# Kernel optimization log

Hardware: AMD Instinct MI355X
Metric: run time of the kernel (lower is better)

The kernel has to match this reference:

```python
import jax, jax.numpy as jnp
import numpy as np

NU, NI, NA, D = 100000, 100000, 10000, 64
N0 = NU + NI        # user+item graph nodes
N1 = NU + NA        # user+author graph nodes
E0, E1, E3, E4, E5 = 6_400_000, 3_520_000, 1_000_000, 1_000_000, 2_000_000
N_LAYERS = 3
EPS = 1e-12


def setup_inputs() -> dict:
    key = jax.random.key(0)
    ks = jax.random.split(key, 18)
    inp = {
        'emb_user': 0.1 * jax.random.normal(ks[0], (NU, D), jnp.float32),
        'emb_item': 0.1 * jax.random.normal(ks[1], (NI, D), jnp.float32),
        'emb_author': 0.1 * jax.random.normal(ks[2], (NA, D), jnp.float32),
        'g0_row': jax.random.randint(ks[3], (E0,), 0, N0, jnp.int32),
        'g0_col': jax.random.randint(ks[4], (E0,), 0, N0, jnp.int32),
        'g0_val': jax.random.uniform(ks[5], (E0,), jnp.float32) / 32.0,
        'g1_row': jax.random.randint(ks[6], (E1,), 0, N1, jnp.int32),
        'g1_col': jax.random.randint(ks[7], (E1,), 0, N1, jnp.int32),
        'g1_val': jax.random.uniform(ks[8], (E1,), jnp.float32) / 32.0,
        'g3_row': jax.random.randint(ks[9], (E3,), 0, NA, jnp.int32),
        'g3_col': jax.random.randint(ks[10], (E3,), 0, NI, jnp.int32),
        'g3_val': jax.random.uniform(ks[11], (E3,), jnp.float32),
        'g4_row': jax.random.randint(ks[12], (E4,), 0, NI, jnp.int32),
        'g4_col': jax.random.randint(ks[13], (E4,), 0, NA, jnp.int32),
        'g4_val': jax.random.uniform(ks[14], (E4,), jnp.float32),
        'g5_row': jax.random.randint(ks[15], (E5,), 0, NI, jnp.int32),
        'g5_col': jax.random.randint(ks[16], (E5,), 0, NI, jnp.int32),
        'g5_val': jax.random.uniform(ks[17], (E5,), jnp.float32),
    }
    return inp


def _spmm(row, col, val, x, n):
    # sparse [n, m] @ dense [m, d] via gather + segment_sum
    return jax.ops.segment_sum(val[:, None] * x[col], row, num_segments=n)


def _normalize(x):
    # F.normalize(x, p=2, dim=1)
    return x / jnp.maximum(jnp.linalg.norm(x, axis=1, keepdims=True), EPS)


def _one_propagate(row, col, val, a, b, n):
    # LightGCN propagation: stack per-layer features, mean across layers
    feats = jnp.concatenate([a, b], axis=0)  # [n, D]
    acc = feats
    cur = feats
    for _ in range(N_LAYERS):
        cur = _spmm(row, col, val, cur, n)
        acc = acc + cur
    out = acc / (N_LAYERS + 1)
    return out[: a.shape[0]], out[a.shape[0]:]


def reference(emb_user, emb_item, emb_author,
              g0_row, g0_col, g0_val,
              g1_row, g1_col, g1_val,
              g3_row, g3_col, g3_val,
              g4_row, g4_col, g4_val,
              g5_row, g5_col, g5_val):
    # atom branch: user-item graph
    atom_users, atom_items0 = _one_propagate(g0_row, g0_col, g0_val, emb_user, emb_item, N0)
    atom_authors = _normalize(_spmm(g3_row, g3_col, g3_val, atom_items0, NA))
    atom_items = 0.5 * _normalize(_spmm(g5_row, g5_col, g5_val, atom_items0, NI)) + 0.5 * atom_items0
    # non-atom branch: user-author graph
    non_atom_users, non_atom_authors = _one_propagate(g1_row, g1_col, g1_val, emb_user, emb_author, N1)
    non_atom_items = _normalize(_spmm(g4_row, g4_col, g4_val, non_atom_authors, NI))
    # computer() returns ([u0,u1],[i0,i1],[a0,a1]); concat to one array for a single baseline output
    return jnp.concatenate([atom_users, non_atom_users,
                            atom_items, non_atom_items,
                            atom_authors, non_atom_authors], axis=0)
```

## Files before the change

### kernel.cpp

```cpp
#include <hip/hip_runtime.h>

#define NUu 100000
#define NIi 100000
#define NAa 10000
#define DD  64
#define NN0 (NUu + NIi)
#define NN1 (NUu + NAa)

typedef unsigned int uint;
typedef unsigned short ushort;


__device__ __forceinline__ uint pack_bf2(float x, float y) {
    uint a = __float_as_uint(x);
    uint b = __float_as_uint(y);
    a = (a + 0x7fffu + ((a >> 16) & 1u)) >> 16;
    b = (b + 0x7fffu + ((b >> 16) & 1u)) & 0xffff0000u;
    return (a & 0xffffu) | b;
}
__device__ __forceinline__ float bflo(uint w) { return __uint_as_float(w << 16); }
__device__ __forceinline__ float bfhi(uint w) { return __uint_as_float(w & 0xffff0000u); }

__device__ __forceinline__ uint enc14(float v) {
    uint u = __float_as_uint(v);
    uint bf = (u + 0x7fffu + ((u >> 16) & 1u)) >> 16;
    return ((bf + 1u) >> 1) & 0x3FFFu;
}
__device__ __forceinline__ float dec14(uint e) { return __uint_as_float(e << 17); }

__global__ void k_f2bf3(const float4* __restrict__ su, const float4* __restrict__ si,
                        const float4* __restrict__ sa,
                        uint2* __restrict__ du, uint2* __restrict__ di,
                        uint2* __restrict__ da) {
    int i = blockIdx.x * blockDim.x + threadIdx.x;
    const int nu = NUu * 16, ni = NIi * 16, na = NAa * 16;
    const float4* s;
    uint2* d;
    int j;
    if (i < nu) { s = su; d = du; j = i; }
    else if (i < nu + ni) { s = si; d = di; j = i - nu; }
    else if (i < nu + ni + na) { s = sa; d = da; j = i - nu - ni; }
    else return;
    float4 v = s[j];
    uint2 o;
    o.x = pack_bf2(v.x, v.y);
    o.y = pack_bf2(v.z, v.w);
    d[j] = o;
}


#define P1_ITER 8
#define SEG_CAP 9472

__global__ void k_arenainit(int* __restrict__ bc,
                            int nb0, int nb1, int nb2, int nb3, int nb4,
                            int c0, int c1, int c2, int c3, int c4) {
    int t = threadIdx.x;
    if (t < nb0) bc[t] = t * c0;
    if (t < nb1) bc[1024 + t] = t * c1;
    if (t < nb2) bc[2048 + t] = t * c2;
    if (t < nb3) bc[3072 + t] = t * c3;
    if (t < nb4) bc[4096 + t] = t * c4;
}

__global__ void __launch_bounds__(1024)
k_part1(const int* __restrict__ row, const int* __restrict__ col,
        const float* __restrict__ val, int* __restrict__ binCur,
        int2* __restrict__ stage, int E, int shift, int nbins, int cap) {
    __shared__ int h[1024];
    for (int t = threadIdx.x; t < nbins; t += blockDim.x) h[t] = 0;
    __syncthreads();
    int e0 = blockIdx.x * (blockDim.x * P1_ITER) + threadIdx.x;
    int r[P1_ITER];
#pragma unroll
    for (int i = 0; i < P1_ITER; ++i) {
        int e = e0 + i * blockDim.x;
        r[i] = (e < E) ? row[e] : -1;
        if (r[i] >= 0) atomicAdd(&h[r[i] >> shift], 1);
    }
    __syncthreads();
    for (int t = threadIdx.x; t < nbins; t += blockDim.x) {
        int c = h[t];
        h[t] = c ? atomicAdd(binCur + t, c) : 0;
    }
    __syncthreads();
#pragma unroll
    for (int i = 0; i < P1_ITER; ++i) {
        int e = e0 + i * blockDim.x;
        if (e < E) {
            int rr = r[i];
            int b = rr >> shift;
            int pos = atomicAdd(&h[b], 1);
            if (pos < (b + 1) * cap) {
                int2 p;
                p.x = ((rr & ((1 << shift) - 1)) << 18) | col[e];
                p.y = __float_as_int(val[e]);
                stage[pos] = p;
            }
        }
    }
}

__global__ void __launch_bounds__(1024)
k_part2(const int* __restrict__ binCur, const int2* __restrict__ stage,
        uint* __restrict__ csr, int2* __restrict__ rp2, int N, int shift, int cap) {
    __shared__ int2 seg[SEG_CAP];
    __shared__ int h[512];
    __shared__ int s[512];
    int tid = threadIdx.x;
    int rbase = blockIdx.x << shift;
    int nr = min(1 << shift, N - rbase);
    int es = blockIdx.x * cap;
    int ee = min(binCur[blockIdx.x], es + cap);
    int n = ee - es;
    if (tid < 512) h[tid] = 0;
    for (int i = tid; i < n; i += blockDim.x) seg[i] = stage[es + i];
    __syncthreads();
    for (int i = tid; i < n; i += blockDim.x)
        atomicAdd(&h[seg[i].x >> 18], 1);
    __syncthreads();
    int v = (tid < 512) ? h[tid] : 0;
    if (tid < 512) s[tid] = v;
    __syncthreads();
    for (int off = 1; off < 512; off <<= 1) {
        int t = (tid < 512 && tid >= off) ? s[tid - off] : 0;
        __syncthreads();
        if (tid < 512) s[tid] += t;
        __syncthreads();
    }
    if (tid < 512) h[tid] = es + s[tid] - v;
    if (tid < nr) {
        int st = es + s[tid] - v;
        rp2[rbase + tid] = make_int2(st, st + v);
    }
    __syncthreads();
    for (int i = tid; i < n; i += blockDim.x) {
        int2 p = seg[i];
        int pos = atomicAdd(&h[p.x >> 18], 1);
        csr[pos] = (((uint)(p.x & 0x3ffff)) << 14) | enc14(__int_as_float(p.y));
    }
}


template <bool SS>
__device__ __forceinline__ const uint* gb(uint pe, const uint* xbA, const uint* xbB,
                                          int split) {
    int c = (int)(pe >> 14);
    if (SS) return (c < split) ? xbA + (((long long)c) << 5)
                               : xbB + (((long long)(c - split)) << 5);
    return xbA + (((long long)c) << 5);
}

template <int MODE, bool SS>
__global__ void k_spmm(const int2* __restrict__ rp2, const uint* __restrict__ csr,
                       const uint* __restrict__ xbA, const uint* __restrict__ xbB, int split,
                       const float* __restrict__ embA, const float* __restrict__ embB,
                       const uint* __restrict__ y1b, const uint* __restrict__ y2b,
                       float* __restrict__ outU, float* __restrict__ outI,
                       uint* __restrict__ outIb,
                       uint* __restrict__ ob, float* __restrict__ yf,
                       const float* __restrict__ base, int nrows) {
    int r = blockIdx.x * (blockDim.x >> 6) + (threadIdx.x >> 6);
    if (r >= nrows) return;
    int lane = threadIdx.x & 63;
    int q = lane >> 4;
    int d8 = lane & 15;

    int2 se = rp2[r];
    int s0 = se.x, e0 = se.y;
    float a0 = 0.f, a1 = 0.f, a2 = 0.f, a3 = 0.f;
    int i = s0;
    for (; i + 32 <= e0; i += 32) {
        uint pe[8];
#pragma unroll
        for (int s = 0; s < 8; ++s)
            pe[s] = csr[i + 4 * s + q];
        uint2 wv[8];
#pragma unroll
        for (int s = 0; s < 8; ++s)
            wv[s] = *(const uint2*)(gb<SS>(pe[s], xbA, xbB, split) + 2 * d8);
#pragma unroll
        for (int s = 0; s < 8; ++s) {
            float v = dec14(pe[s] & 0x3FFFu);
            a0 += v * bflo(wv[s].x); a1 += v * bfhi(wv[s].x);
            a2 += v * bflo(wv[s].y); a3 += v * bfhi(wv[s].y);
        }
    }
    for (; i + 8 <= e0; i += 8) {
        uint p0 = csr[i + q];
        uint p1 = csr[i + 4 + q];
        uint2 w0 = *(const uint2*)(gb<SS>(p0, xbA, xbB, split) + 2 * d8);
        uint2 w1 = *(const uint2*)(gb<SS>(p1, xbA, xbB, split) + 2 * d8);
        float v0 = dec14(p0 & 0x3FFFu);
        float v1 = dec14(p1 & 0x3FFFu);
        a0 += v0 * bflo(w0.x); a1 += v0 * bfhi(w0.x);
        a2 += v0 * bflo(w0.y); a3 += v0 * bfhi(w0.y);
        a0 += v1 * bflo(w1.x); a1 += v1 * bfhi(w1.x);
        a2 += v1 * bflo(w1.y); a3 += v1 * bfhi(w1.y);
    }
    for (; i < e0; i += 4) {
        int idx = i + q;
        uint pe = (idx < e0) ? csr[idx] : 0u;
        uint2 wv = *(const uint2*)(gb<SS>(pe, xbA, xbB, split) + 2 * d8);
        float v = dec14(pe & 0x3FFFu);
        a0 += v * bflo(wv.x); a1 += v * bfhi(wv.x); a2 += v * bflo(wv.y); a3 += v * bfhi(wv.y);
    }
    a0 += __shfl_xor(a0, 16); a0 += __shfl_xor(a0, 32);
    a1 += __shfl_xor(a1, 16); a1 += __shfl_xor(a1, 32);
    a2 += __shfl_xor(a2, 16); a2 += __shfl_xor(a2, 32);
    a3 += __shfl_xor(a3, 16); a3 += __shfl_xor(a3, 32);

    long long off4 = (((long long)r) << 6) + 4 * d8;
    long long offw = (((long long)r) << 5) + 2 * d8;

    if (MODE == 0) {
        if (q == 0) {
            uint2 o;
            o.x = pack_bf2(a0, a1);
            o.y = pack_bf2(a2, a3);
            *(uint2*)(ob + offw) = o;
        }
    } else if (MODE == 1) {
        if (q == 0) {
            float4 e4;
            if (r < split) e4 = *(const float4*)(embA + off4);
            else           e4 = *(const float4*)(embB + (off4 - (((long long)split) << 6)));
            uint2 w1 = *(const uint2*)(y1b + offw);
            uint2 w2 = *(const uint2*)(y2b + offw);
            float s0f = 0.25f * (e4.x + bflo(w1.x) + bflo(w2.x) + a0);
            float s1f = 0.25f * (e4.y + bfhi(w1.x) + bfhi(w2.x) + a1);
            float s2f = 0.25f * (e4.z + bflo(w1.y) + bflo(w2.y) + a2);
            float s3f = 0.25f * (e4.w + bfhi(w1.y) + bfhi(w2.y) + a3);
            float4 o;
            o.x = s0f; o.y = s1f; o.z = s2f; o.w = s3f;
            if (r < split) {
                *(float4*)(outU + off4) = o;
            } else {
                *(float4*)(outI + (off4 - (((long long)split) << 6))) = o;
                if (outIb) {
                    uint2 ob2;
                    ob2.x = pack_bf2(s0f, s1f);
                    ob2.y = pack_bf2(s2f, s3f);
                    *(uint2*)(outIb + (((long long)(r - split)) << 5) + 2 * d8) = ob2;
                }
            }
        }
    } else {
        float sq = a0 * a0 + a1 * a1 + a2 * a2 + a3 * a3;
        sq += __shfl_xor(sq, 1); sq += __shfl_xor(sq, 2);
        sq += __shfl_xor(sq, 4); sq += __shfl_xor(sq, 8);
        float inv = 1.0f / fmaxf(sqrtf(sq), 1e-12f);
        if (q == 0) {
            float4 o;
            if (MODE == 2) {
                o.x = a0 * inv; o.y = a1 * inv; o.z = a2 * inv; o.w = a3 * inv;
            } else {
                float4 b4 = *(const float4*)(base + off4);
                o.x = 0.5f * a0 * inv + 0.5f * b4.x;
                o.y = 0.5f * a1 * inv + 0.5f * b4.y;
                o.z = 0.5f * a2 * inv + 0.5f * b4.z;
                o.w = 0.5f * a3 * inv + 0.5f * b4.w;
            }
            *(float4*)(yf + off4) = o;
        }
    }
}


static inline int nblk(long long n, int b) { return (int)((n + b - 1) / b); }
static inline size_t al256(size_t x) { return (x + 255) & ~(size_t)255; }
#define AMAX 7250000

extern "C" void kernel_launch(void* const* d_in, const int* in_sizes, int n_in,
                              void* d_out, int out_size, void* d_ws, size_t ws_size,
                              hipStream_t stream) {
    const float* emb_user   = (const float*)d_in[0];
    const float* emb_item   = (const float*)d_in[1];
    const float* emb_author = (const float*)d_in[2];
    const int*   g0r = (const int*)d_in[3];
    const int*   g0c = (const int*)d_in[4];
    const float* g0v = (const float*)d_in[5];
    const int*   g1r = (const int*)d_in[6];
    const int*   g1c = (const int*)d_in[7];
    const float* g1v = (const float*)d_in[8];
    const int*   g3r = (const int*)d_in[9];
    const int*   g3c = (const int*)d_in[10];
    const float* g3v = (const float*)d_in[11];
    const int*   g4r = (const int*)d_in[12];
    const int*   g4c = (const int*)d_in[13];
    const float* g4v = (const float*)d_in[14];
    const int*   g5r = (const int*)d_in[15];
    const int*   g5c = (const int*)d_in[16];
    const float* g5v = (const float*)d_in[17];

    const int E0 = in_sizes[3];
    const int E1 = in_sizes[6];
    const int E3 = in_sizes[9];
    const int E4 = in_sizes[12];
    const int E5 = in_sizes[15];

    float* out = (float*)d_out;

    char* w = (char*)d_ws;
    int2* rp2     = (int2*)w; w += al256((size_t)(NN0 + 1) * 8);
    int*  binCur5 = (int*)w;  w += al256((size_t)5 * 1024 * 4);
    uint* csr     = (uint*)w; w += al256((size_t)AMAX * 4);
    uint* embUb   = (uint*)w; w += al256((size_t)NUu * 32 * 4);
    uint* embIb   = (uint*)w; w += al256((size_t)NIi * 32 * 4);
    uint* embAb   = (uint*)w; w += al256((size_t)NAa * 32 * 4);
    uint* y1b     = (uint*)w; w += al256((size_t)NN0 * 32 * 4);
    uint* y2b     = (uint*)w; w += al256((size_t)NN0 * 32 * 4);
    uint* items0b = (uint*)w; w += al256((size_t)NIi * 32 * 4);
    float* items0 = (float*)w; w += al256((size_t)NIi * DD * 4);
    uint* oAuthNb = (uint*)w; w += al256((size_t)NAa * 32 * 4);
    int2* stage = (int2*)y1b;

    const int B = 256;

    struct G { int nbins, shift, cap; };
    auto geo = [](int E, int N, int shift) {
        G g;
        g.shift = shift;
        g.nbins = (N + (1 << shift) - 1) >> shift;
        int cap = E / g.nbins + E / (16 * g.nbins) + 512;
        g.cap = cap > SEG_CAP ? SEG_CAP : cap;
        return g;
    };
    G gg0 = geo(E0, NN0, 8), gg1 = geo(E1, NN1, 8), gg3 = geo(E3, NAa, 5),
      gg5 = geo(E5, NIi, 8), gg4 = geo(E4, NIi, 8);

    float* oUserA = out;
    float* oUserN = out + (long long)NUu * DD;
    float* oItemA = out + (long long)200000 * DD;
    float* oItemN = out + (long long)300000 * DD;
    float* oAuthA = out + (long long)400000 * DD;
    float* oAuthN = out + (long long)410000 * DD;

    k_f2bf3<<<nblk((long long)(NUu + NIi + NAa) * 16, B), B, 0, stream>>>(
        (const float4*)emb_user, (const float4*)emb_item, (const float4*)emb_author,
        (uint2*)embUb, (uint2*)embIb, (uint2*)embAb);
    k_arenainit<<<1, 1024, 0, stream>>>(binCur5,
        gg0.nbins, gg1.nbins, gg3.nbins, gg5.nbins, gg4.nbins,
        gg0.cap, gg1.cap, gg3.cap, gg5.cap, gg4.cap);

    auto build = [&](const int* row, const int* col, const float* val,
                     int E, int N, const G& g, int slot) {
        int* bc = binCur5 + slot * 1024;
        k_part1<<<nblk(E, 1024 * P1_ITER), 1024, 0, stream>>>(row, col, val, bc,
                                                              stage, E, g.shift,
                                                              g.nbins, g.cap);
        k_part2<<<g.nbins, 1024, 0, stream>>>(bc, stage, csr, rp2, N, g.shift, g.cap);
    };

    build(g0r, g0c, g0v, E0, NN0, gg0, 0);
    k_spmm<0, true><<<nblk(NN0, 4), B, 0, stream>>>(rp2, csr, embUb, embIb, NUu,
                                                    nullptr, nullptr, nullptr, nullptr,
                                                    nullptr, nullptr, nullptr,
                                                    y1b, nullptr, nullptr, NN0);
    k_spmm<0, false><<<nblk(NN0, 4), B, 0, stream>>>(rp2, csr, y1b, nullptr, 0,
                                                     nullptr, nullptr, nullptr, nullptr,
                                                     nullptr, nullptr, nullptr,
                                                     y2b, nullptr, nullptr, NN0);
    k_spmm<1, false><<<nblk(NN0, 4), B, 0, stream>>>(rp2, csr, y2b, nullptr, NUu,
                                                     emb_user, emb_item, y1b, y2b,
                                                     oUserA, items0, items0b,
                                                     nullptr, nullptr, nullptr, NN0);

    build(g1r, g1c, g1v, E1, NN1, gg1, 1);
    k_spmm<0, true><<<nblk(NN1, 4), B, 0, stream>>>(rp2, csr, embUb, embAb, NUu,
                                                    nullptr, nullptr, nullptr, nullptr,
                                                    nullptr, nullptr, nullptr,
                                                    y1b, nullptr, nullptr, NN1);
    k_spmm<0, false><<<nblk(NN1, 4), B, 0, stream>>>(rp2, csr, y1b, nullptr, 0,
                                                     nullptr, nullptr, nullptr, nullptr,
                                                     nullptr, nullptr, nullptr,
                                                     y2b, nullptr, nullptr, NN1);
    k_spmm<1, false><<<nblk(NN1, 4), B, 0, stream>>>(rp2, csr, y2b, nullptr, NUu,
                                                     emb_user, emb_author, y1b, y2b,
                                                     oUserN, oAuthN, oAuthNb,
                                                     nullptr, nullptr, nullptr, NN1);

    build(g3r, g3c, g3v, E3, NAa, gg3, 2);
    k_spmm<2, false><<<nblk(NAa, 4), B, 0, stream>>>(rp2, csr, items0b, nullptr, 0,
                                                     nullptr, nullptr, nullptr, nullptr,
                                                     nullptr, nullptr, nullptr,
                                                     nullptr, oAuthA, nullptr, NAa);

    build(g5r, g5c, g5v, E5, NIi, gg5, 3);
    k_spmm<3, false><<<nblk(NIi, 4), B, 0, stream>>>(rp2, csr, items0b, nullptr, 0,
                                                     nullptr, nullptr, nullptr, nullptr,
                                                     nullptr, nullptr, nullptr,
                                                     nullptr, oItemA, items0, NIi);

    build(g4r, g4c, g4v, E4, NIi, gg4, 4);
    k_spmm<2, false><<<nblk(NIi, 4), B, 0, stream>>>(rp2, csr, oAuthNb, nullptr, 0,
                                                     nullptr, nullptr, nullptr, nullptr,
                                                     nullptr, nullptr, nullptr,
                                                     nullptr, oItemN, nullptr, NIi);
}
```

Baseline: 1.076 ms.

## Split LightGCN propagation into two 32-column halves for cache-resident gathers

The bf16 embeddings and intermediate layer buffers are stored as two separate 32-column halves, and each 3-layer propagation runs twice, once per half, with a new half-width SpMM kernel. Halving the gathered row footprint is meant to let the randomly accessed source matrix fit better in L2/LLC and cut gather traffic. In exchange, the CSR index and value stream is read twice as often, kernel launches double, and each gather is now a 4-byte load per lane instead of 8.

```diff
diff --git a/kernel.cpp b/kernel.cpp
--- a/kernel.cpp
+++ b/kernel.cpp
@@ -28,24 +28,27 @@
 }
 __device__ __forceinline__ float dec14(uint e) { return __uint_as_float(e << 17); }
 
-__global__ void k_f2bf3(const float4* __restrict__ su, const float4* __restrict__ si,
-                        const float4* __restrict__ sa,
-                        uint2* __restrict__ du, uint2* __restrict__ di,
-                        uint2* __restrict__ da) {
+__global__ void k_f2bf3s(const float4* __restrict__ su, const float4* __restrict__ si,
+                         const float4* __restrict__ sa,
+                         uint2* __restrict__ ulo, uint2* __restrict__ uhi,
+                         uint2* __restrict__ ilo, uint2* __restrict__ ihi,
+                         uint2* __restrict__ alo, uint2* __restrict__ ahi) {
     int i = blockIdx.x * blockDim.x + threadIdx.x;
     const int nu = NUu * 16, ni = NIi * 16, na = NAa * 16;
     const float4* s;
-    uint2* d;
+    uint2 *dlo, *dhi;
     int j;
-    if (i < nu) { s = su; d = du; j = i; }
-    else if (i < nu + ni) { s = si; d = di; j = i - nu; }
-    else if (i < nu + ni + na) { s = sa; d = da; j = i - nu - ni; }
+    if (i < nu) { s = su; dlo = ulo; dhi = uhi; j = i; }
+    else if (i < nu + ni) { s = si; dlo = ilo; dhi = ihi; j = i - nu; }
+    else if (i < nu + ni + na) { s = sa; dlo = alo; dhi = ahi; j = i - nu - ni; }
     else return;
     float4 v = s[j];
     uint2 o;
     o.x = pack_bf2(v.x, v.y);
     o.y = pack_bf2(v.z, v.w);
-    d[j] = o;
+    int n = j >> 4, k = j & 15;
+    uint2* d = (k < 8) ? dlo : dhi;
+    d[n * 8 + (k & 7)] = o;
 }
 
 
@@ -141,25 +144,101 @@
     }
 }
 
-
-template <bool SS>
-__device__ __forceinline__ const uint* gb(uint pe, const uint* xbA, const uint* xbB,
-                                          int split) {
-    int c = (int)(pe >> 14);
-    if (SS) return (c < split) ? xbA + (((long long)c) << 5)
-                               : xbB + (((long long)(c - split)) << 5);
-    return xbA + (((long long)c) << 5);
-}
-
 template <int MODE, bool SS>
+__global__ void k_spmmh(const int2* __restrict__ rp2, const uint* __restrict__ csr,
+                        const uint* __restrict__ xbA, const uint* __restrict__ xbB,
+                        int split, int dOff,
+                        const float* __restrict__ embA, const float* __restrict__ embB,
+                        const uint* __restrict__ y1p, const uint* __restrict__ y2p,
+                        float* __restrict__ outU, float* __restrict__ outI,
+                        uint* __restrict__ outIb, uint* __restrict__ yp, int nrows) {
+    int r = blockIdx.x * (blockDim.x >> 6) + (threadIdx.x >> 6);
+    if (r >= nrows) return;
+    int lane = threadIdx.x & 63;
+    int q = lane >> 4;
+    int d8 = lane & 15;
+
+    int2 se = rp2[r];
+    int s0 = se.x, e0 = se.y;
+    float a0 = 0.f, a1 = 0.f;
+    int i = s0;
+    for (; i + 32 <= e0; i += 32) {
+        uint pe[8];
+#pragma unroll
+        for (int s = 0; s < 8; ++s)
+            pe[s] = csr[i + 4 * s + q];
+        uint wv[8];
+#pragma unroll
+        for (int s = 0; s < 8; ++s) {
+            int c = (int)(pe[s] >> 14);
+            const uint* b = SS ? ((c < split) ? xbA + (((long long)c) << 4)
+                                             : xbB + (((long long)(c - split)) << 4))
+                               : xbA + (((long long)c) << 4);
+            wv[s] = b[d8];
+        }
+#pragma unroll
+        for (int s = 0; s < 8; ++s) {
+            float v = dec14(pe[s] & 0x3FFFu);
+            a0 += v * bflo(wv[s]); a1 += v * bfhi(wv[s]);
+        }
+    }
+    for (; i + 8 <= e0; i += 8) {
+        uint p0 = csr[i + q];
+        uint p1 = csr[i + 4 + q];
+        int c0 = (int)(p0 >> 14), c1 = (int)(p1 >> 14);
+        const uint* b0 = SS ? ((c0 < split) ? xbA + (((long long)c0) << 4)
+                                            : xbB + (((long long)(c0 - split)) << 4))
+                            : xbA + (((long long)c0) << 4);
+        const uint* b1 = SS ? ((c1 < split) ? xbA + (((long long)c1) << 4)
+                                            : xbB + (((long long)(c1 - split)) << 4))
+                            : xbA + (((long long)c1) << 4);
+        uint w0 = b0[d8], w1 = b1[d8];
+        float v0 = dec14(p0 & 0x3FFFu);
+        float v1 = dec14(p1 & 0x3FFFu);
+        a0 += v0 * bflo(w0); a1 += v0 * bfhi(w0);
+        a0 += v1 * bflo(w1); a1 += v1 * bfhi(w1);
+    }
+    for (; i < e0; i += 4) {
+        int idx = i + q;
+        uint pe = (idx < e0) ? csr[idx] : 0u;
+        int c = (int)(pe >> 14);
+        const uint* b = SS ? ((c < split) ? xbA + (((long long)c) << 4)
+                                          : xbB + (((long long)(c - split)) << 4))
+                           : xbA + (((long long)c) << 4);
+        uint w = b[d8];
+        float v = dec14(pe & 0x3FFFu);
+        a0 += v * bflo(w); a1 += v * bfhi(w);
+    }
+    a0 += __shfl_xor(a0, 16); a0 += __shfl_xor(a0, 32);
+    a1 += __shfl_xor(a1, 16); a1 += __shfl_xor(a1, 32);
+
+    if (q != 0) return;
+    if (MODE == 0) {
+        yp[(((long long)r) << 4) + d8] = pack_bf2(a0, a1);
+    } else {
+        long long offf = (((long long)r) << 6) + dOff + 2 * d8;
+        float2 e2;
+        if (r < split) e2 = *(const float2*)(embA + offf);
+        else           e2 = *(const float2*)(embB + (offf - (((long long)split) << 6)));
+        uint w1 = y1p[(((long long)r) << 4) + d8];
+        uint w2 = y2p[(((long long)r) << 4) + d8];
+        float s0f = 0.25f * (e2.x + bflo(w1) + bflo(w2) + a0);
+        float s1f = 0.25f * (e2.y + bfhi(w1) + bfhi(w2) + a1);
+        float2 o; o.x = s0f; o.y = s1f;
+        if (r < split) {
+            *(float2*)(outU + offf) = o;
+        } else {
+            *(float2*)(outI + (offf - (((long long)split) << 6))) = o;
+            if (outIb)
+                outIb[(((long long)(r - split)) << 5) + (dOff >> 1) + d8] = pack_bf2(s0f, s1f);
+        }
+    }
+}
+
+template <int MODE>
 __global__ void k_spmm(const int2* __restrict__ rp2, const uint* __restrict__ csr,
-                       const uint* __restrict__ xbA, const uint* __restrict__ xbB, int split,
-                       const float* __restrict__ embA, const float* __restrict__ embB,
-                       const uint* __restrict__ y1b, const uint* __restrict__ y2b,
-                       float* __restrict__ outU, float* __restrict__ outI,
-                       uint* __restrict__ outIb,
-                       uint* __restrict__ ob, float* __restrict__ yf,
-                       const float* __restrict__ base, int nrows) {
+                       const uint* __restrict__ xb,
+                       float* __restrict__ yf, const float* __restrict__ base, int nrows) {
     int r = blockIdx.x * (blockDim.x >> 6) + (threadIdx.x >> 6);
     if (r >= nrows) return;
     int lane = threadIdx.x & 63;
@@ -178,7 +257,7 @@
         uint2 wv[8];
 #pragma unroll
         for (int s = 0; s < 8; ++s)
-            wv[s] = *(const uint2*)(gb<SS>(pe[s], xbA, xbB, split) + 2 * d8);
+            wv[s] = *(const uint2*)(xb + (((long long)(pe[s] >> 14)) << 5) + 2 * d8);
 #pragma unroll
         for (int s = 0; s < 8; ++s) {
             float v = dec14(pe[s] & 0x3FFFu);
@@ -186,22 +265,10 @@
             a2 += v * bflo(wv[s].y); a3 += v * bfhi(wv[s].y);
         }
     }
-    for (; i + 8 <= e0; i += 8) {
-        uint p0 = csr[i + q];
-        uint p1 = csr[i + 4 + q];
-        uint2 w0 = *(const uint2*)(gb<SS>(p0, xbA, xbB, split) + 2 * d8);
-        uint2 w1 = *(const uint2*)(gb<SS>(p1, xbA, xbB, split) + 2 * d8);
-        float v0 = dec14(p0 & 0x3FFFu);
-        float v1 = dec14(p1 & 0x3FFFu);
-        a0 += v0 * bflo(w0.x); a1 += v0 * bfhi(w0.x);
-        a2 += v0 * bflo(w0.y); a3 += v0 * bfhi(w0.y);
-        a0 += v1 * bflo(w1.x); a1 += v1 * bfhi(w1.x);
-        a2 += v1 * bflo(w1.y); a3 += v1 * bfhi(w1.y);
-    }
     for (; i < e0; i += 4) {
         int idx = i + q;
         uint pe = (idx < e0) ? csr[idx] : 0u;
-        uint2 wv = *(const uint2*)(gb<SS>(pe, xbA, xbB, split) + 2 * d8);
+        uint2 wv = *(const uint2*)(xb + (((long long)(pe >> 14)) << 5) + 2 * d8);
         float v = dec14(pe & 0x3FFFu);
         a0 += v * bflo(wv.x); a1 += v * bfhi(wv.x); a2 += v * bflo(wv.y); a3 += v * bfhi(wv.y);
     }
@@ -210,59 +277,23 @@
     a2 += __shfl_xor(a2, 16); a2 += __shfl_xor(a2, 32);
     a3 += __shfl_xor(a3, 16); a3 += __shfl_xor(a3, 32);
 
-    long long off4 = (((long long)r) << 6) + 4 * d8;
-    long long offw = (((long long)r) << 5) + 2 * d8;
-
-    if (MODE == 0) {
-        if (q == 0) {
-            uint2 o;
-            o.x = pack_bf2(a0, a1);
-            o.y = pack_bf2(a2, a3);
-            *(uint2*)(ob + offw) = o;
-        }
-    } else if (MODE == 1) {
-        if (q == 0) {
-            float4 e4;
-            if (r < split) e4 = *(const float4*)(embA + off4);
-            else           e4 = *(const float4*)(embB + (off4 - (((long long)split) << 6)));
-            uint2 w1 = *(const uint2*)(y1b + offw);
-            uint2 w2 = *(const uint2*)(y2b + offw);
-            float s0f = 0.25f * (e4.x + bflo(w1.x) + bflo(w2.x) + a0);
-            float s1f = 0.25f * (e4.y + bfhi(w1.x) + bfhi(w2.x) + a1);
-            float s2f = 0.25f * (e4.z + bflo(w1.y) + bflo(w2.y) + a2);
-            float s3f = 0.25f * (e4.w + bfhi(w1.y) + bfhi(w2.y) + a3);
-            float4 o;
-            o.x = s0f; o.y = s1f; o.z = s2f; o.w = s3f;
-            if (r < split) {
-                *(float4*)(outU + off4) = o;
-            } else {
-                *(float4*)(outI + (off4 - (((long long)split) << 6))) = o;
-                if (outIb) {
-                    uint2 ob2;
-                    ob2.x = pack_bf2(s0f, s1f);
-                    ob2.y = pack_bf2(s2f, s3f);
-                    *(uint2*)(outIb + (((long long)(r - split)) << 5) + 2 * d8) = ob2;
-                }
-            }
-        }
-    } else {
-        float sq = a0 * a0 + a1 * a1 + a2 * a2 + a3 * a3;
-        sq += __shfl_xor(sq, 1); sq += __shfl_xor(sq, 2);
-        sq += __shfl_xor(sq, 4); sq += __shfl_xor(sq, 8);
-        float inv = 1.0f / fmaxf(sqrtf(sq), 1e-12f);
-        if (q == 0) {
-            float4 o;
-            if (MODE == 2) {
-                o.x = a0 * inv; o.y = a1 * inv; o.z = a2 * inv; o.w = a3 * inv;
-            } else {
-                float4 b4 = *(const float4*)(base + off4);
-                o.x = 0.5f * a0 * inv + 0.5f * b4.x;
-                o.y = 0.5f * a1 * inv + 0.5f * b4.y;
-                o.z = 0.5f * a2 * inv + 0.5f * b4.z;
-                o.w = 0.5f * a3 * inv + 0.5f * b4.w;
-            }
-            *(float4*)(yf + off4) = o;
-        }
+    float sq = a0 * a0 + a1 * a1 + a2 * a2 + a3 * a3;
+    sq += __shfl_xor(sq, 1); sq += __shfl_xor(sq, 2);
+    sq += __shfl_xor(sq, 4); sq += __shfl_xor(sq, 8);
+    float inv = 1.0f / fmaxf(sqrtf(sq), 1e-12f);
+    if (q == 0) {
+        long long off4 = (((long long)r) << 6) + 4 * d8;
+        float4 o;
+        if (MODE == 2) {
+            o.x = a0 * inv; o.y = a1 * inv; o.z = a2 * inv; o.w = a3 * inv;
+        } else {
+            float4 b4 = *(const float4*)(base + off4);
+            o.x = 0.5f * a0 * inv + 0.5f * b4.x;
+            o.y = 0.5f * a1 * inv + 0.5f * b4.y;
+            o.z = 0.5f * a2 * inv + 0.5f * b4.z;
+            o.w = 0.5f * a3 * inv + 0.5f * b4.w;
+        }
+        *(float4*)(yf + off4) = o;
     }
 }
 
@@ -315,6 +346,12 @@
     uint* oAuthNb = (uint*)w; w += al256((size_t)NAa * 32 * 4);
     int2* stage = (int2*)y1b;
 
+    uint* embU_p[2] = { embUb, embUb + (size_t)NUu * 16 };
+    uint* embI_p[2] = { embIb, embIb + (size_t)NIi * 16 };
+    uint* embA_p[2] = { embAb, embAb + (size_t)NAa * 16 };
+    uint* y1_p[2]   = { y1b,  y1b + (size_t)NN0 * 16 };
+    uint* y2_p[2]   = { y2b,  y2b + (size_t)NN0 * 16 };
+
     const int B = 256;
 
     struct G { int nbins, shift, cap; };
@@ -336,9 +373,11 @@
     float* oAuthA = out + (long long)400000 * DD;
     float* oAuthN = out + (long long)410000 * DD;
 
-    k_f2bf3<<<nblk((long long)(NUu + NIi + NAa) * 16, B), B, 0, stream>>>(
+    k_f2bf3s<<<nblk((long long)(NUu + NIi + NAa) * 16, B), B, 0, stream>>>(
         (const float4*)emb_user, (const float4*)emb_item, (const float4*)emb_author,
-        (uint2*)embUb, (uint2*)embIb, (uint2*)embAb);
+        (uint2*)embU_p[0], (uint2*)embU_p[1],
+        (uint2*)embI_p[0], (uint2*)embI_p[1],
+        (uint2*)embA_p[0], (uint2*)embA_p[1]);
     k_arenainit<<<1, 1024, 0, stream>>>(binCur5,
         gg0.nbins, gg1.nbins, gg3.nbins, gg5.nbins, gg4.nbins,
         gg0.cap, gg1.cap, gg3.cap, gg5.cap, gg4.cap);
@@ -352,49 +391,38 @@
         k_part2<<<g.nbins, 1024, 0, stream>>>(bc, stage, csr, rp2, N, g.shift, g.cap);
     };
 
+    auto propagate = [&](uint* eA_p0, uint* eA_p1, uint* eB_p0, uint* eB_p1,
+                         const float* fA, const float* fB,
+                         float* oU, float* oI, uint* oIb, int N) {
+        uint* eA_p[2] = { eA_p0, eA_p1 };
+        uint* eB_p[2] = { eB_p0, eB_p1 };
+        for (int p = 0; p < 2; ++p) {
+            k_spmmh<0, true><<<nblk(N, 4), B, 0, stream>>>(rp2, csr,
+                eA_p[p], eB_p[p], NUu, 32 * p, nullptr, nullptr,
+                nullptr, nullptr, nullptr, nullptr, nullptr, y1_p[p], N);
+            k_spmmh<0, false><<<nblk(N, 4), B, 0, stream>>>(rp2, csr,
+                y1_p[p], nullptr, 0, 32 * p, nullptr, nullptr,
+                nullptr, nullptr, nullptr, nullptr, nullptr, y2_p[p], N);
+            k_spmmh<1, false><<<nblk(N, 4), B, 0, stream>>>(rp2, csr,
+                y2_p[p], nullptr, NUu, 32 * p, fA, fB,
+                y1_p[p], y2_p[p], oU, oI, oIb, nullptr, N);
+        }
+    };
+
     build(g0r, g0c, g0v, E0, NN0, gg0, 0);
-    k_spmm<0, true><<<nblk(NN0, 4), B, 0, stream>>>(rp2, csr, embUb, embIb, NUu,
-                                                    nullptr, nullptr, nullptr, nullptr,
-                                                    nullptr, nullptr, nullptr,
-                                                    y1b, nullptr, nullptr, NN0);
-    k_spmm<0, false><<<nblk(NN0, 4), B, 0, stream>>>(rp2, csr, y1b, nullptr, 0,
-                                                     nullptr, nullptr, nullptr, nullptr,
-                                                     nullptr, nullptr, nullptr,
-                                                     y2b, nullptr, nullptr, NN0);
-    k_spmm<1, false><<<nblk(NN0, 4), B, 0, stream>>>(rp2, csr, y2b, nullptr, NUu,
-                                                     emb_user, emb_item, y1b, y2b,
-                                                     oUserA, items0, items0b,
-                                                     nullptr, nullptr, nullptr, NN0);
+    propagate(embU_p[0], embU_p[1], embI_p[0], embI_p[1],
+              emb_user, emb_item, oUserA, items0, items0b, NN0);
 
     build(g1r, g1c, g1v, E1, NN1, gg1, 1);
-    k_spmm<0, true><<<nblk(NN1, 4), B, 0, stream>>>(rp2, csr, embUb, embAb, NUu,
-                                                    nullptr, nullptr, nullptr, nullptr,
-                                                    nullptr, nullptr, nullptr,
-                                                    y1b, nullptr, nullptr, NN1);
-    k_spmm<0, false><<<nblk(NN1, 4), B, 0, stream>>>(rp2, csr, y1b, nullptr, 0,
-                                                     nullptr, nullptr, nullptr, nullptr,
-                                                     nullptr, nullptr, nullptr,
-                                                     y2b, nullptr, nullptr, NN1);
-    k_spmm<1, false><<<nblk(NN1, 4), B, 0, stream>>>(rp2, csr, y2b, nullptr, NUu,
-                                                     emb_user, emb_author, y1b, y2b,
-                                                     oUserN, oAuthN, oAuthNb,
-                                                     nullptr, nullptr, nullptr, NN1);
+    propagate(embU_p[0], embU_p[1], embA_p[0], embA_p[1],
+              emb_user, emb_author, oUserN, oAuthN, oAuthNb, NN1);
 
     build(g3r, g3c, g3v, E3, NAa, gg3, 2);
-    k_spmm<2, false><<<nblk(NAa, 4), B, 0, stream>>>(rp2, csr, items0b, nullptr, 0,
-                                                     nullptr, nullptr, nullptr, nullptr,
-                                                     nullptr, nullptr, nullptr,
-                                                     nullptr, oAuthA, nullptr, NAa);
+    k_spmm<2><<<nblk(NAa, 4), B, 0, stream>>>(rp2, csr, items0b, oAuthA, nullptr, NAa);
 
     build(g5r, g5c, g5v, E5, NIi, gg5, 3);
-    k_spmm<3, false><<<nblk(NIi, 4), B, 0, stream>>>(rp2, csr, items0b, nullptr, 0,
-                                                     nullptr, nullptr, nullptr, nullptr,
-                                                     nullptr, nullptr, nullptr,
-                                                     nullptr, oItemA, items0, NIi);
+    k_spmm<3><<<nblk(NIi, 4), B, 0, stream>>>(rp2, csr, items0b, oItemA, items0, NIi);
 
     build(g4r, g4c, g4v, E4, NIi, gg4, 4);
-    k_spmm<2, false><<<nblk(NIi, 4), B, 0, stream>>>(rp2, csr, oAuthNb, nullptr, 0,
-                                                     nullptr, nullptr, nullptr, nullptr,
-                                                     nullptr, nullptr, nullptr,
-                                                     nullptr, oItemN, nullptr, NIi);
-}
+    k_spmm<2><<<nblk(NIi, 4), B, 0, stream>>>(rp2, csr, oAuthNb, oItemN, nullptr, NIi);
+}
```

Result: slower. 1.513 ms (+40.6%).
